# Kernel tuning notes

Measured on AMD Instinct MI355X. Metric: run time of the kernel, lower is better.

The kernel has to match this reference:

```python
import jax, jax.numpy as jnp
import numpy as np

H, HEAD_DIM = 12, 64
D = H * HEAD_DIM  # 768
SCALE = HEAD_DIM ** -0.5


def setup_inputs() -> dict:
    key = jax.random.key(0)
    ks = jax.random.split(key, 8)
    B, N, M, C = 2, 2048, 2048, 768
    s = 0.02
    return {
        "x": jax.random.normal(ks[0], (B, N, C), jnp.float32),
        "src": jax.random.normal(ks[1], (B, M, C), jnp.float32),
        "qk_w": jax.random.normal(ks[2], (2 * D, C), jnp.float32) * s,
        "qk_src_w": jax.random.normal(ks[3], (2 * D, C), jnp.float32) * s,
        "v_w": jax.random.normal(ks[4], (D, C), jnp.float32) * s,
        "v_src_w": jax.random.normal(ks[5], (D, C), jnp.float32) * s,
        "proj_w": jax.random.normal(ks[6], (C, D), jnp.float32) * s,
        "proj_b": jnp.zeros((C,), jnp.float32),
        "proj_src_w": jax.random.normal(ks[7], (C, D), jnp.float32) * s,
        "proj_src_b": jnp.zeros((C,), jnp.float32),
    }


def reference(x, src, qk_w, qk_src_w, v_w, v_src_w, proj_w, proj_b, proj_src_w, proj_src_b):
    B, N, _ = x.shape
    M = src.shape[1]

    def split_heads(t):  # [B, L, H*dh] -> [B, H, L, dh]
        return t.reshape(B, -1, H, t.shape[-1] // H).transpose(0, 2, 1, 3)

    qk = split_heads(x @ qk_w.T)          # [B,H,N,2*HEAD_DIM]
    qk_s = split_heads(src @ qk_src_w.T)  # [B,H,M,2*HEAD_DIM]
    v = split_heads(x @ v_w.T)            # [B,H,N,HEAD_DIM]
    v_s = split_heads(src @ v_src_w.T)    # [B,H,M,HEAD_DIM]

    # shared similarity: computed once, softmaxed along both directions
    sim = jnp.einsum('bhnd,bhmd->bhnm', qk * SCALE, qk_s)  # [B,H,N,M]
    attn = jax.nn.softmax(sim, axis=-1)      # x -> src (rows)
    attn_src = jax.nn.softmax(sim, axis=-2)  # src -> x (columns)

    y = jnp.einsum('bhnm,bhmd->bhnd', attn, v_s)       # [B,H,N,dh]
    y_src = jnp.einsum('bhnm,bhnd->bhmd', attn_src, v)  # [B,H,M,dh]

    merge = lambda t: t.transpose(0, 2, 1, 3).reshape(B, -1, D)
    y = merge(y) @ proj_w.T + proj_b
    y_src = merge(y_src) @ proj_src_w.T + proj_src_b
    return jnp.concatenate([y, y_src], axis=-1)  # [B, N, out+out_src]
```

## Files before the change

kernel.cpp:

```cpp
#include <hip/hip_runtime.h>
#include <hip/hip_bf16.h>
#include <cstdint>
#include <cstddef>


typedef __attribute__((ext_vector_type(4))) float f32x4;
typedef __attribute__((ext_vector_type(8))) short bf16x8;
typedef __attribute__((ext_vector_type(4))) short s16x4;
typedef __attribute__((ext_vector_type(4))) unsigned int u32x4;

__device__ __forceinline__ short f2bf(float f) {
  union { float f; unsigned u; } v; v.f = f;
  unsigned r = v.u + 0x7FFF + ((v.u >> 16) & 1);
  return (short)(r >> 16);
}

__device__ __forceinline__ unsigned cvt_pk_bf16(float lo, float hi) {
  unsigned r;
  asm("v_cvt_pk_bf16_f32 %0, %1, %2" : "=v"(r) : "v"(lo), "v"(hi));
  return r;
}

__device__ __forceinline__ void async16(const void* g, void* l) {
  __builtin_amdgcn_global_load_lds(
      (__attribute__((address_space(1))) unsigned int*)(g),
      (__attribute__((address_space(3))) unsigned int*)(l),
      16, 0, 0);
}

__global__ __launch_bounds__(256)
void cvt_all(const float* __restrict__ x, const float* __restrict__ src,
             const float* __restrict__ qkw, const float* __restrict__ qksw,
             const float* __restrict__ vw, const float* __restrict__ vsw,
             const float* __restrict__ pw, const float* __restrict__ psw,
             short* __restrict__ out) {
  int i = blockIdx.x * 256 + threadIdx.x;
  const float* in; int local; float scale = 1.f;
  if (i < 1572864) {
    if (i < 786432) { in = x; local = i; } else { in = src; local = i - 786432; }
  } else if (i < 2162688) {
    if (i < 1867776) { in = qkw; local = i - 1572864; scale = 0.125f * 1.44269504f; }
    else             { in = qksw; local = i - 1867776; }
  } else if (i < 2457600) {
    if (i < 2310144) { in = vw; local = i - 2162688; } else { in = vsw; local = i - 2310144; }
  } else {
    if (i < 2605056) { in = pw; local = i - 2457600; } else { in = psw; local = i - 2605056; }
  }
  float4 v = ((const float4*)in)[local];
  s16x4 o = { f2bf(v.x * scale), f2bf(v.y * scale),
              f2bf(v.z * scale), f2bf(v.w * scale) };
  ((s16x4*)out)[i] = o;
}

enum { EPI_HEAD128 = 0, EPI_HEADT64 = 1, EPI_PROJ = 2 };

template<int EPI>
__global__ __launch_bounds__(256)
void gemm_bt2(const short* __restrict__ A0, const short* __restrict__ W0,
              short* __restrict__ ob0, const float* __restrict__ bias0,
              const short* __restrict__ A1, const short* __restrict__ W1,
              short* __restrict__ ob1, const float* __restrict__ bias1,
              float* __restrict__ outf) {
  __shared__ short As[128 * 32];
  __shared__ short Ws[128 * 32];

  const int sel = blockIdx.y >> 5;
  const int by  = blockIdx.y & 31;
  const short* A = sel ? A1 : A0;
  const short* W = sel ? W1 : W0;
  short* outb = sel ? ob1 : ob0;
  const float* bias = sel ? bias1 : bias0;
  const int outColOff = sel ? 768 : 0;

  const int tid  = threadIdx.x;
  const int lane = tid & 63, wid = tid >> 6;
  const int wr = wid >> 1, wc = wid & 1;
  const int rowBase = by << 7, colBase = blockIdx.x << 7;
  const int c = lane & 15, g = lane >> 4;

  const short* gA = A + (size_t)(rowBase + wid * 32 + (lane >> 2)) * 768 + (lane & 3) * 8;
  const short* gW = W + (size_t)(colBase + wid * 32 + (lane >> 2)) * 768 + (lane & 3) * 8;
  short* lA = As + wid * 32 * 32;
  short* lW = Ws + wid * 32 * 32;

  const short* rA = As + (wr * 64 + c) * 32 + g * 8;
  const short* rW = Ws + (wc * 64 + c) * 32 + g * 8;

  f32x4 acc[4][4] = {};

  for (int kt = 0; kt < 24; ++kt) {
    async16(gA,            lA);
    async16(gA + 16 * 768, lA + 16 * 32);
    async16(gW,            lW);
    async16(gW + 16 * 768, lW + 16 * 32);
    gA += 32; gW += 32;
    __syncthreads();
    bf16x8 af[4], wf[4];
#pragma unroll
    for (int i = 0; i < 4; ++i) af[i] = *(const bf16x8*)(rA + i * 512);
#pragma unroll
    for (int j = 0; j < 4; ++j) wf[j] = *(const bf16x8*)(rW + j * 512);
#pragma unroll
    for (int i = 0; i < 4; ++i)
#pragma unroll
      for (int j = 0; j < 4; ++j)
        acc[i][j] = __builtin_amdgcn_mfma_f32_16x16x32_bf16(af[i], wf[j], acc[i][j], 0, 0, 0);
    __syncthreads();
  }

  if (EPI == EPI_HEAD128) {
#pragma unroll
    for (int i = 0; i < 4; ++i) {
      int row = rowBase + wr * 64 + i * 16 + g * 4;
      int b = row >> 11, n = row & 2047;
#pragma unroll
      for (int j = 0; j < 4; ++j) {
        int f = colBase + wc * 64 + j * 16 + c;
        int h = f >> 7, d = f & 127;
        short* p = outb + ((size_t)(b * 12 + h) * 2048 + n) * 128 + d;
#pragma unroll
        for (int r = 0; r < 4; ++r) p[(size_t)r * 128] = f2bf(acc[i][j][r]);
      }
    }
  } else if (EPI == EPI_HEADT64) {
#pragma unroll
    for (int i = 0; i < 4; ++i) {
      int row = rowBase + wr * 64 + i * 16 + g * 4;
      int b = row >> 11, n = row & 2047;
#pragma unroll
      for (int j = 0; j < 4; ++j) {
        int f = colBase + wc * 64 + j * 16 + c;
        int h = f >> 6, d = f & 63;
        s16x4 o4 = { f2bf(acc[i][j][0]), f2bf(acc[i][j][1]),
                     f2bf(acc[i][j][2]), f2bf(acc[i][j][3]) };
        *(s16x4*)(outb + ((size_t)(b * 12 + h) * 64 + d) * 2048 + n) = o4;
      }
    }
  } else {
#pragma unroll
    for (int j = 0; j < 4; ++j) {
      int colj = colBase + wc * 64 + j * 16 + c;
      float bv = bias[colj];
#pragma unroll
      for (int i = 0; i < 4; ++i) {
        int row = rowBase + wr * 64 + i * 16 + g * 4;
#pragma unroll
        for (int r = 0; r < 4; ++r)
          outf[(size_t)(row + r) * 1536 + outColOff + colj] = acc[i][j][r] + bv;
      }
    }
  }
}

__global__ __launch_bounds__(256)
void attn_fwd(const short* __restrict__ Q0, const short* __restrict__ K0,
              const short* __restrict__ Vt0, short* __restrict__ Y0,
              const short* __restrict__ Q1, const short* __restrict__ K1,
              const short* __restrict__ Vt1, short* __restrict__ Y1) {
  __shared__ short Ks[64 * 136];
  __shared__ short Vs[64 * 72];

  const int dir = blockIdx.y >= 24;
  const int bh  = dir ? blockIdx.y - 24 : blockIdx.y;
  const short* Qg  = dir ? Q1 : Q0;
  const short* Kg  = dir ? K1 : K0;
  const short* Vtg = dir ? Vt1 : Vt0;
  short* Y         = dir ? Y1 : Y0;

  const int tid = threadIdx.x, lane = tid & 63, wid = tid >> 6;
  const int c = lane & 15, g = lane >> 4;
  const int b = bh / 12, h = bh % 12;
  const int q0 = blockIdx.x * 128 + wid * 32;

  bf16x8 qf[2][4];
#pragma unroll
  for (int qb = 0; qb < 2; ++qb) {
    const short* qp = Qg + ((size_t)bh * 2048 + q0 + qb * 16 + c) * 128 + g * 8;
#pragma unroll
    for (int kk = 0; kk < 4; ++kk) qf[qb][kk] = *(const bf16x8*)(qp + kk * 32);
  }

  f32x4 o[2][4];
#pragma unroll
  for (int qb = 0; qb < 2; ++qb)
#pragma unroll
    for (int db = 0; db < 4; ++db) o[qb][db] = f32x4{0.f, 0.f, 0.f, 0.f};
  float lsumP[2] = {0.f, 0.f};

  const short* kbase = Kg + (size_t)bh * 2048 * 128;
  const short* vbase = Vtg + (size_t)bh * 64 * 2048;

  const int srow = tid >> 2, scc = (tid & 3) * 32, skc = (tid & 3) * 16;

  bf16x8 kreg[4], vreg[2];
  auto gload = [&](int kt) {
    const short* srcK = kbase + ((size_t)(kt * 64 + srow)) * 128 + scc;
#pragma unroll
    for (int u = 0; u < 4; ++u) kreg[u] = *(const bf16x8*)(srcK + u * 8);
    const short* srcV = vbase + (size_t)srow * 2048 + kt * 64 + skc;
    vreg[0] = *(const bf16x8*)(srcV);
    vreg[1] = *(const bf16x8*)(srcV + 8);
  };
  auto lwrite = [&]() {
    short* dstK = Ks + srow * 136 + scc;
#pragma unroll
    for (int u = 0; u < 4; ++u) *(bf16x8*)(dstK + u * 8) = kreg[u];
    short* dstV = Vs + srow * 72 + skc;
    *(bf16x8*)(dstV)     = vreg[0];
    *(bf16x8*)(dstV + 8) = vreg[1];
  };

  gload(0);
  for (int kt = 0; kt < 32; ++kt) {
    lwrite();
    __syncthreads();

    f32x4 st[2][4];
#pragma unroll
    for (int qb = 0; qb < 2; ++qb)
#pragma unroll
      for (int j = 0; j < 4; ++j) st[qb][j] = f32x4{0.f, 0.f, 0.f, 0.f};
#pragma unroll
    for (int j = 0; j < 4; ++j)
#pragma unroll
      for (int kk = 0; kk < 4; ++kk) {
        bf16x8 kf = *(const bf16x8*)(Ks + (j * 16 + c) * 136 + kk * 32 + g * 8);
        st[0][j] = __builtin_amdgcn_mfma_f32_16x16x32_bf16(kf, qf[0][kk], st[0][j], 0, 0, 0);
        st[1][j] = __builtin_amdgcn_mfma_f32_16x16x32_bf16(kf, qf[1][kk], st[1][j], 0, 0, 0);
      }

    bf16x8 pa[2][2];
#pragma unroll
    for (int qb = 0; qb < 2; ++qb) {
      float p[4][4];
#pragma unroll
      for (int j = 0; j < 4; ++j)
#pragma unroll
        for (int r = 0; r < 4; ++r) p[j][r] = exp2f(st[qb][j][r]);
      float s0 = (p[0][0] + p[0][1]) + (p[0][2] + p[0][3]);
      float s1 = (p[1][0] + p[1][1]) + (p[1][2] + p[1][3]);
      float s2 = (p[2][0] + p[2][1]) + (p[2][2] + p[2][3]);
      float s3 = (p[3][0] + p[3][1]) + (p[3][2] + p[3][3]);
      lsumP[qb] += (s0 + s1) + (s2 + s3);
#pragma unroll
      for (int kb = 0; kb < 2; ++kb) {
        union { u32x4 u; bf16x8 v; } pk;
        pk.u[0] = cvt_pk_bf16(p[2 * kb][0],     p[2 * kb][1]);
        pk.u[1] = cvt_pk_bf16(p[2 * kb][2],     p[2 * kb][3]);
        pk.u[2] = cvt_pk_bf16(p[2 * kb + 1][0], p[2 * kb + 1][1]);
        pk.u[3] = cvt_pk_bf16(p[2 * kb + 1][2], p[2 * kb + 1][3]);
        pa[qb][kb] = pk.v;
      }
    }

    if (kt + 1 < 32) gload(kt + 1);

#pragma unroll
    for (int kb = 0; kb < 2; ++kb)
#pragma unroll
      for (int db = 0; db < 4; ++db) {
        union { s16x4 h[2]; bf16x8 v; } vf;
        const short* vrow = Vs + (size_t)(db * 16 + c) * 72 + kb * 32 + g * 4;
        vf.h[0] = *(const s16x4*)(vrow);
        vf.h[1] = *(const s16x4*)(vrow + 16);
        o[0][db] = __builtin_amdgcn_mfma_f32_16x16x32_bf16(pa[0][kb], vf.v, o[0][db], 0, 0, 0);
        o[1][db] = __builtin_amdgcn_mfma_f32_16x16x32_bf16(pa[1][kb], vf.v, o[1][db], 0, 0, 0);
      }
    __syncthreads();
  }

  float L[2];
#pragma unroll
  for (int qb = 0; qb < 2; ++qb) {
    float v = lsumP[qb];
    v += __shfl_xor(v, 16, 64);
    v += __shfl_xor(v, 32, 64);
    L[qb] = v;
  }
#pragma unroll
  for (int qb = 0; qb < 2; ++qb) {
    float inv[4];
#pragma unroll
    for (int r = 0; r < 4; ++r)
      inv[r] = 1.0f / __shfl(L[qb], g * 4 + r, 64);
    short* yp = Y + ((size_t)(b * 2048) + q0 + qb * 16 + g * 4) * 768 + h * 64 + c;
#pragma unroll
    for (int db = 0; db < 4; ++db)
#pragma unroll
      for (int r = 0; r < 4; ++r)
        yp[(size_t)r * 768 + db * 16] = f2bf(o[qb][db][r] * inv[r]);
  }
}

extern "C" void kernel_launch(void* const* d_in, const int* in_sizes, int n_in,
                              void* d_out, int out_size, void* d_ws, size_t ws_size,
                              hipStream_t stream) {
  (void)in_sizes; (void)n_in; (void)out_size; (void)ws_size;

  const float* x     = (const float*)d_in[0];
  const float* srcp  = (const float*)d_in[1];
  const float* qk_w  = (const float*)d_in[2];
  const float* qks_w = (const float*)d_in[3];
  const float* v_w   = (const float*)d_in[4];
  const float* vs_w  = (const float*)d_in[5];
  const float* p_w   = (const float*)d_in[6];
  const float* p_b   = (const float*)d_in[7];
  const float* ps_w  = (const float*)d_in[8];
  const float* ps_b  = (const float*)d_in[9];
  float* out = (float*)d_out;

  char* ws = (char*)d_ws;
  size_t off = 0;
  auto alloc = [&](size_t elems) -> short* {
    short* p = (short*)(ws + off);
    off += (elems * 2 + 255) & ~(size_t)255;
    return p;
  };
  short* xb    = alloc(4096UL * 768);
  short* sb    = alloc(4096UL * 768);
  short* qkwb  = alloc(1536UL * 768);
  short* qkswb = alloc(1536UL * 768);
  short* vwb   = alloc(768UL * 768);
  short* vswb  = alloc(768UL * 768);
  short* pwb   = alloc(768UL * 768);
  short* pswb  = alloc(768UL * 768);
  short* qk    = alloc(24UL * 2048 * 128);
  short* qks   = alloc(24UL * 2048 * 128);
  short* vT    = alloc(24UL * 64 * 2048);
  short* vsT   = alloc(24UL * 64 * 2048);
  short* y     = alloc(4096UL * 768);
  short* ysv   = alloc(4096UL * 768);

  cvt_all<<<dim3(10752), dim3(256), 0, stream>>>(x, srcp, qk_w, qks_w, v_w, vs_w,
                                                 p_w, ps_w, xb);

  gemm_bt2<EPI_HEAD128><<<dim3(12, 64), 256, 0, stream>>>(
      xb, qkwb, qk, nullptr, sb, qkswb, qks, nullptr, nullptr);
  gemm_bt2<EPI_HEADT64><<<dim3(6, 64), 256, 0, stream>>>(
      xb, vwb, vT, nullptr, sb, vswb, vsT, nullptr, nullptr);

  attn_fwd<<<dim3(16, 48), 256, 0, stream>>>(qk, qks, vsT, y,
                                             qks, qk, vT, ysv);

  gemm_bt2<EPI_PROJ><<<dim3(6, 64), 256, 0, stream>>>(
      y, pwb, nullptr, p_b, ysv, pswb, nullptr, ps_b, out);
}
```

Before: 202.2 us.

## Load K fragments directly from global, remap blocks per XCD, raise occupancy hint

The K tile is no longer staged through shared memory. Each wave now loads its K MFMA fragments straight from global memory every iteration, which cuts LDS usage and the LDS write and read traffic. Blocks are remapped so that all query tiles of a given (batch, head, direction) land on the same XCD, so repeated K/V reads can hit that XCD's L2. A launch-bounds occupancy hint of 3 blocks is also added. The cost is that every wave now issues redundant global K loads, and this adds memory latency that is no longer prefetched.

```diff
diff --git a/kernel.cpp b/kernel.cpp
--- a/kernel.cpp
+++ b/kernel.cpp
@@ -152,16 +152,21 @@
   }
 }
 
-__global__ __launch_bounds__(256)
+__global__ __launch_bounds__(256, 3)
 void attn_fwd(const short* __restrict__ Q0, const short* __restrict__ K0,
               const short* __restrict__ Vt0, short* __restrict__ Y0,
               const short* __restrict__ Q1, const short* __restrict__ K1,
               const short* __restrict__ Vt1, short* __restrict__ Y1) {
-  __shared__ short Ks[64 * 136];
   __shared__ short Vs[64 * 72];
 
-  const int dir = blockIdx.y >= 24;
-  const int bh  = dir ? blockIdx.y - 24 : blockIdx.y;
+  const int bid  = blockIdx.y * 16 + blockIdx.x;
+  const int xcd  = bid & 7;
+  const int slot = bid >> 3;
+  const int bhd  = xcd * 6 + (slot >> 4);
+  const int qi   = slot & 15;
+
+  const int dir = bhd >= 24;
+  const int bh  = dir ? bhd - 24 : bhd;
   const short* Qg  = dir ? Q1 : Q0;
   const short* Kg  = dir ? K1 : K0;
   const short* Vtg = dir ? Vt1 : Vt0;
@@ -170,7 +175,7 @@
   const int tid = threadIdx.x, lane = tid & 63, wid = tid >> 6;
   const int c = lane & 15, g = lane >> 4;
   const int b = bh / 12, h = bh % 12;
-  const int q0 = blockIdx.x * 128 + wid * 32;
+  const int q0 = qi * 128 + wid * 32;
 
   bf16x8 qf[2][4];
 #pragma unroll
@@ -190,31 +195,37 @@
   const short* kbase = Kg + (size_t)bh * 2048 * 128;
   const short* vbase = Vtg + (size_t)bh * 64 * 2048;
 
-  const int srow = tid >> 2, scc = (tid & 3) * 32, skc = (tid & 3) * 16;
-
-  bf16x8 kreg[4], vreg[2];
-  auto gload = [&](int kt) {
-    const short* srcK = kbase + ((size_t)(kt * 64 + srow)) * 128 + scc;
-#pragma unroll
-    for (int u = 0; u < 4; ++u) kreg[u] = *(const bf16x8*)(srcK + u * 8);
+  const int srow = tid >> 2, skc = (tid & 3) * 16;
+
+  const short* kfrag = kbase + (size_t)c * 128 + g * 8;
+
+  bf16x8 vreg[2];
+  auto gloadV = [&](int kt) {
     const short* srcV = vbase + (size_t)srow * 2048 + kt * 64 + skc;
     vreg[0] = *(const bf16x8*)(srcV);
     vreg[1] = *(const bf16x8*)(srcV + 8);
   };
-  auto lwrite = [&]() {
-    short* dstK = Ks + srow * 136 + scc;
-#pragma unroll
-    for (int u = 0; u < 4; ++u) *(bf16x8*)(dstK + u * 8) = kreg[u];
+  auto lwriteV = [&]() {
     short* dstV = Vs + srow * 72 + skc;
     *(bf16x8*)(dstV)     = vreg[0];
     *(bf16x8*)(dstV + 8) = vreg[1];
   };
 
-  gload(0);
+  gloadV(0);
   for (int kt = 0; kt < 32; ++kt) {
-    lwrite();
+    lwriteV();
     __syncthreads();
 
+    bf16x8 kf[4][4];
+    {
+      const short* kp = kfrag + (size_t)(kt * 64) * 128;
+#pragma unroll
+      for (int j = 0; j < 4; ++j)
+#pragma unroll
+        for (int kk = 0; kk < 4; ++kk)
+          kf[j][kk] = *(const bf16x8*)(kp + (size_t)(j * 16) * 128 + kk * 32);
+    }
+
     f32x4 st[2][4];
 #pragma unroll
     for (int qb = 0; qb < 2; ++qb)
@@ -224,9 +235,8 @@
     for (int j = 0; j < 4; ++j)
 #pragma unroll
       for (int kk = 0; kk < 4; ++kk) {
-        bf16x8 kf = *(const bf16x8*)(Ks + (j * 16 + c) * 136 + kk * 32 + g * 8);
-        st[0][j] = __builtin_amdgcn_mfma_f32_16x16x32_bf16(kf, qf[0][kk], st[0][j], 0, 0, 0);
-        st[1][j] = __builtin_amdgcn_mfma_f32_16x16x32_bf16(kf, qf[1][kk], st[1][j], 0, 0, 0);
+        st[0][j] = __builtin_amdgcn_mfma_f32_16x16x32_bf16(kf[j][kk], qf[0][kk], st[0][j], 0, 0, 0);
+        st[1][j] = __builtin_amdgcn_mfma_f32_16x16x32_bf16(kf[j][kk], qf[1][kk], st[1][j], 0, 0, 0);
       }
 
     bf16x8 pa[2][2];
@@ -253,7 +263,7 @@
       }
     }
 
-    if (kt + 1 < 32) gload(kt + 1);
+    if (kt + 1 < 32) gloadV(kt + 1);
 
 #pragma unroll
     for (int kb = 0; kb < 2; ++kb)
```

Measured after the change: 282.1 us. +39.5%, slower.
